# Performance work log

Hardware: AMD Instinct MI355X
Metric: run time of the kernel (lower is better)

## Reference

```python
import jax, jax.numpy as jnp
import numpy as np

B = 16
C = 80
LEVELS = [(128, 128, 8), (64, 64, 16), (32, 32, 32), (16, 16, 64), (8, 8, 128)]
TOPN = 1000
MIN_SCORE = 0.05
NMS_THR = 0.6
MAX_OBJ = 100


def setup_inputs() -> dict:
    key = jax.random.key(0)
    inp = {}
    for l, (H, W, s) in enumerate(LEVELS):
        key, k1, k2, k3 = jax.random.split(key, 4)
        inp[f"cls{l}"] = jax.random.uniform(k1, (B, H, W, C), jnp.float32)
        inp[f"reg{l}"] = jax.random.uniform(k2, (B, H, W, 4), jnp.float32) * 128.0
        inp[f"ctr{l}"] = jax.random.uniform(k3, (B, H, W, 1), jnp.float32)
        xs = (jnp.arange(W, dtype=jnp.float32) + 0.5) * s
        ys = (jnp.arange(H, dtype=jnp.float32) + 0.5) * s
        gx, gy = jnp.meshgrid(xs, ys)  # [H, W]
        pos = jnp.stack([gx, gy], axis=-1)  # [H, W, 2]
        inp[f"pos{l}"] = jnp.broadcast_to(pos, (B, H, W, 2))
    return inp


def _nms_one(scores, classes, bboxes):
    # scores [N], classes int32 [N], bboxes float [N, 4] (already int-truncated values)
    s = jnp.where(scores > MIN_SCORE, scores, -jnp.inf)  # score-threshold mask
    top_s, top_i = jax.lax.top_k(s, TOPN)  # sort descending, keep topn
    top_c = jax.lax.stop_gradient(classes[top_i].astype(jnp.float32))
    top_b = bboxes[top_i]
    valid = top_s > MIN_SCORE
    wh = top_b[:, 2:4] - top_b[:, 0:2]
    areas = jnp.clip(wh[:, 0] * wh[:, 1], 0.0001)
    ar = jnp.arange(TOPN)

    def body(i, suppressed):
        active = valid[i] & (~suppressed[i])
        b = top_b[i]
        tl = jnp.maximum(b[0:2], top_b[:, 0:2])
        br = jnp.minimum(b[2:4], top_b[:, 2:4])
        owh = jnp.clip(br - tl, 0.0)
        inter = owh[:, 0] * owh[:, 1]
        union = jnp.clip(areas[i] + areas - inter, 0.0001)
        iou = inter / union
        return suppressed | (active & (ar > i) & (iou >= NMS_THR))

    suppressed = jax.lax.fori_loop(0, TOPN, body, jnp.zeros((TOPN,), bool))
    keep = valid & (~suppressed)
    rank = jnp.cumsum(keep.astype(jnp.int32)) - 1
    # scatter kept detections (in score order) into first MAX_OBJ slots; slot MAX_OBJ is a dump
    idx = jnp.where(keep & (rank < MAX_OBJ), rank, MAX_OBJ)
    out_s = jnp.full((MAX_OBJ + 1,), -1.0, jnp.float32).at[idx].set(jnp.where(keep, top_s, -1.0))[:MAX_OBJ]
    out_c = jnp.full((MAX_OBJ + 1,), -1.0, jnp.float32).at[idx].set(jnp.where(keep, top_c, -1.0))[:MAX_OBJ]
    out_b = jnp.zeros((MAX_OBJ + 1, 4), jnp.float32).at[idx].set(jnp.where(keep[:, None], top_b, 0.0))[:MAX_OBJ]
    return out_s, out_c, out_b


def _forward(cls_list, reg_list, ctr_list, pos_list):
    ss, cc, bb = [], [], []
    for c, r, t, p in zip(cls_list, reg_list, ctr_list, pos_list):
        b = c.shape[0]
        c = c.reshape(b, -1, c.shape[-1])   # [B, HW, 80]
        r = r.reshape(b, -1, 4)             # [B, HW, 4]
        t = t.reshape(b, -1)                # [B, HW]
        p = p.reshape(b, -1, 2)             # [B, HW, 2]
        sc = jnp.sqrt(jnp.max(c, axis=2) * t)
        cl = jnp.argmax(c, axis=2).astype(jnp.int32)
        bmin = p - r[:, :, 0:2]
        bmax = p + r[:, :, 2:4]
        # torch .int() truncates toward zero; values are used as floats afterward
        box = jax.lax.stop_gradient(jnp.trunc(jnp.concatenate([bmin, bmax], axis=2)))
        ss.append(sc); cc.append(cl); bb.append(box)
    scores = jnp.concatenate(ss, axis=1)
    classes = jnp.concatenate(cc, axis=1)
    boxes = jnp.concatenate(bb, axis=1)
    return jax.vmap(_nms_one)(scores, classes, boxes)


def reference(cls0, cls1, cls2, cls3, cls4, reg0, reg1, reg2, reg3, reg4,
              ctr0, ctr1, ctr2, ctr3, ctr4, pos0, pos1, pos2, pos3, pos4):
    return _forward([cls0, cls1, cls2, cls3, cls4],
                    [reg0, reg1, reg2, reg3, reg4],
                    [ctr0, ctr1, ctr2, ctr3, ctr4],
                    [pos0, pos1, pos2, pos3, pos4])
```

## Files before the change

### kernel.cpp

```cpp
#include <hip/hip_runtime.h>
#include <stdint.h>

typedef unsigned int u32;
typedef unsigned long long u64;

#define NTOT 21824
#define NBATCH 16
#define TOPN 1000
#define MAXOBJ 100
#define CAP 2048
#define CAPC 8192

__global__ __launch_bounds__(256) void decode_kernel(
    const float* __restrict__ cls0, const float* __restrict__ cls1,
    const float* __restrict__ cls2, const float* __restrict__ cls3,
    const float* __restrict__ cls4,
    const float* __restrict__ ctr0, const float* __restrict__ ctr1,
    const float* __restrict__ ctr2, const float* __restrict__ ctr3,
    const float* __restrict__ ctr4,
    u32* __restrict__ keys, int* __restrict__ clsidx)
{
    int tid = threadIdx.x;
    int g = tid >> 2, j = tid & 3;
    int loc = blockIdx.x * 64 + g;
    int b = blockIdx.y;
    if (loc >= NTOT) return;
    const float *cp, *tp;
    if (loc < 16384)      { size_t o = (size_t)b*16384 + loc;          cp = cls0 + o*80; tp = ctr0 + o; }
    else if (loc < 20480) { size_t o = (size_t)b*4096  + (loc-16384);  cp = cls1 + o*80; tp = ctr1 + o; }
    else if (loc < 21504) { size_t o = (size_t)b*1024  + (loc-20480);  cp = cls2 + o*80; tp = ctr2 + o; }
    else if (loc < 21760) { size_t o = (size_t)b*256   + (loc-21504);  cp = cls3 + o*80; tp = ctr3 + o; }
    else                  { size_t o = (size_t)b*64    + (loc-21760);  cp = cls4 + o*80; tp = ctr4 + o; }

    const float4* c4 = (const float4*)cp;
    float maxv = -1.0f; int arg = 0;
#pragma unroll
    for (int q = 0; q < 5; ++q) {
        float4 v = c4[j + 4*q];
        int ch = 16*q + 4*j;
        if (v.x > maxv) { maxv = v.x; arg = ch;     }
        if (v.y > maxv) { maxv = v.y; arg = ch + 1; }
        if (v.z > maxv) { maxv = v.z; arg = ch + 2; }
        if (v.w > maxv) { maxv = v.w; arg = ch + 3; }
    }
#pragma unroll
    for (int d = 1; d <= 2; d <<= 1) {
        float ov = __shfl_xor(maxv, d);
        int   oa = __shfl_xor(arg, d);
        if (ov > maxv || (ov == maxv && oa < arg)) { maxv = ov; arg = oa; }
    }
    if (j == 0) {
        float score = sqrtf(maxv * (*tp));
        u32 key = (score > 0.05f) ? (__float_as_uint(score) | 0x80000000u) : 0u;
        size_t o = (size_t)b * NTOT + loc;
        keys[o] = key;
        clsidx[o] = arg;
    }
}

__global__ __launch_bounds__(1024) void pivot_kernel(
    const u32* __restrict__ keys,
    u64* __restrict__ cb, u64* __restrict__ cand2,
    u32* __restrict__ gcnt, u32* __restrict__ params,
    float* __restrict__ tscore, float* __restrict__ tcls, float4* __restrict__ tbox)
{
    __shared__ u32 h4[4][2048];
    __shared__ u32 s_wtot[16];
    __shared__ int s_tf;
    __shared__ u32 s_C, s_above, s_cnt;
    int b = blockIdx.x, tid = threadIdx.x;
    int lane = tid & 63, wave = tid >> 6, sub = wave & 3;
    const u32* kb = keys + (size_t)b * NTOT;
    u64* cbb = cb + (size_t)b * CAPC;
    u64* c2b = cand2 + (size_t)b * CAPC;

    for (int i = tid; i < TOPN; i += 1024) {
        size_t o = (size_t)b * TOPN + i;
        tscore[o] = -1.0f; tcls[o] = -1.0f;
        tbox[o] = make_float4(0.f, 0.f, 0.f, 0.f);
    }

    for (int i = tid; i < 4 * 2048; i += 1024) ((u32*)h4)[i] = 0;
    if (tid == 0) { s_tf = -1; s_cnt = 0; }
    __syncthreads();
    for (int i = tid; i < NTOT; i += 1024) {
        u32 k = kb[i];
        if (k) atomicAdd(&h4[sub][k >> 21], 1u);
    }
    __syncthreads();
    u32 h0 = h4[0][2*tid] + h4[1][2*tid] + h4[2][2*tid] + h4[3][2*tid];
    u32 h1 = h4[0][2*tid+1] + h4[1][2*tid+1] + h4[2][2*tid+1] + h4[3][2*tid+1];
    u32 x = h0 + h1;
#pragma unroll
    for (int off = 1; off < 64; off <<= 1) {
        u32 y = __shfl_down(x, off);
        if (lane + off < 64) x += y;
    }
    if (lane == 0) s_wtot[wave] = x;
    __syncthreads();
    u32 wsuf = 0, tot = 0;
    for (int w2 = 0; w2 < 16; ++w2) { u32 v = s_wtot[w2]; tot += v; if (w2 > wave) wsuf += v; }
    u32 suf0 = x + wsuf, suf1 = suf0 - h0;
    u32 target = (tot < TOPN) ? tot : TOPN;
    if (target > 0) {
        if (suf0 >= target) atomicMax(&s_tf, 2 * tid);
        if (suf1 >= target) atomicMax(&s_tf, 2 * tid + 1);
    }
    __syncthreads();
    int t0 = s_tf;
    if (target > 0) {
        if (2 * tid == t0)     { s_C = suf0; s_above = suf0 - h0; }
        if (2 * tid + 1 == t0) { s_C = suf1; s_above = suf1 - h1; }
    }
    __syncthreads();
    u32 C0 = (target > 0) ? s_C : 0;
    u32 above0 = (target > 0) ? s_above : 0;
    bool useCand = (C0 <= CAPC);

    for (int base = 0; base < NTOT; base += 1024) {
        int i = base + tid;
        u32 k = (i < NTOT) ? kb[i] : 0u;
        bool pass = (target > 0) && k && ((int)(k >> 21) >= t0);
        u64 mask = __ballot(pass);
        u32 wcnt = (u32)__popcll(mask);
        u32 wbase = 0;
        if (lane == 0 && wcnt) wbase = atomicAdd(&s_cnt, wcnt);
        wbase = __shfl(wbase, 0);
        if (pass) {
            u32 pos = wbase + (u32)__popcll(mask & ((1ull << lane) - 1ull));
            if (pos < CAPC) cbb[pos] = ((u64)k << 32) | (u32)(~i);
        }
    }
    __syncthreads();
    u32 C0g = s_cnt; (void)C0g;
    __syncthreads();
    if (tid == 0) s_cnt = 0;

    bool need2 = (target > 0 && C0 > CAP);
    int t1 = 0; u32 C1 = 0, above1 = 0;
    for (int i = tid; i < 4 * 2048; i += 1024) ((u32*)h4)[i] = 0;
    if (tid == 0) s_tf = -1;
    __syncthreads();
    if (need2) {
        if (useCand) {
            for (u32 i = tid; i < C0; i += 1024) {
                u32 k = (u32)(cbb[i] >> 32);
                if ((int)(k >> 21) == t0) atomicAdd(&h4[sub][(k >> 10) & 2047], 1u);
            }
        } else {
            for (int i = tid; i < NTOT; i += 1024) {
                u32 k = kb[i];
                if (k && (int)(k >> 21) == t0) atomicAdd(&h4[sub][(k >> 10) & 2047], 1u);
            }
        }
    }
    __syncthreads();
    {
        u32 g0 = h4[0][2*tid] + h4[1][2*tid] + h4[2][2*tid] + h4[3][2*tid];
        u32 g1 = h4[0][2*tid+1] + h4[1][2*tid+1] + h4[2][2*tid+1] + h4[3][2*tid+1];
        u32 x2 = g0 + g1;
#pragma unroll
        for (int off = 1; off < 64; off <<= 1) {
            u32 y = __shfl_down(x2, off);
            if (lane + off < 64) x2 += y;
        }
        if (lane == 0) s_wtot[wave] = x2;
        __syncthreads();
        u32 ws2 = 0;
        for (int w2 = wave + 1; w2 < 16; ++w2) ws2 += s_wtot[w2];
        u32 sa0 = x2 + ws2, sa1 = sa0 - g0;
        u32 need2c = target - above0;
        if (need2) {
            if (sa0 >= need2c) atomicMax(&s_tf, 2 * tid);
            if (sa1 >= need2c) atomicMax(&s_tf, 2 * tid + 1);
        }
        __syncthreads();
        t1 = s_tf;
        if (need2) {
            if (2 * tid == t1)     { s_C = above0 + sa0; s_above = above0 + sa0 - g0; }
            if (2 * tid + 1 == t1) { s_C = above0 + sa1; s_above = above0 + sa1 - g1; }
        }
        __syncthreads();
        if (need2) { C1 = s_C; above1 = s_above; }
    }

    bool need3 = (need2 && C1 > CAP);
    int t2 = 0;
    __syncthreads();
    for (int i = tid; i < 4 * 2048; i += 1024) ((u32*)h4)[i] = 0;
    if (tid == 0) s_tf = -1;
    __syncthreads();
    if (need3) {
        if (useCand) {
            for (u32 i = tid; i < C0; i += 1024) {
                u32 k = (u32)(cbb[i] >> 32);
                if ((int)(k >> 21) == t0 && (int)((k >> 10) & 2047) == t1)
                    atomicAdd(&h4[sub][k & 1023], 1u);
            }
        } else {
            for (int i = tid; i < NTOT; i += 1024) {
                u32 k = kb[i];
                if (k && (int)(k >> 21) == t0 && (int)((k >> 10) & 2047) == t1)
                    atomicAdd(&h4[sub][k & 1023], 1u);
            }
        }
    }
    __syncthreads();
    {
        u32 g0 = h4[0][2*tid] + h4[1][2*tid] + h4[2][2*tid] + h4[3][2*tid];
        u32 g1 = h4[0][2*tid+1] + h4[1][2*tid+1] + h4[2][2*tid+1] + h4[3][2*tid+1];
        u32 x3 = g0 + g1;
#pragma unroll
        for (int off = 1; off < 64; off <<= 1) {
            u32 y = __shfl_down(x3, off);
            if (lane + off < 64) x3 += y;
        }
        if (lane == 0) s_wtot[wave] = x3;
        __syncthreads();
        u32 ws3 = 0;
        for (int w2 = wave + 1; w2 < 16; ++w2) ws3 += s_wtot[w2];
        u32 sb0 = x3 + ws3, sb1 = sb0 - g0;
        if (need3) {
            u32 need3c = target - above1;
            if (sb0 >= need3c) atomicMax(&s_tf, 2 * tid);
            if (sb1 >= need3c) atomicMax(&s_tf, 2 * tid + 1);
        }
        __syncthreads();
        t2 = s_tf;
    }

    u32 P;
    if (target == 0) P = 0xFFFFFFFFu;
    else if (!need2) P = (u32)t0 << 21;
    else if (!need3) P = ((u32)t0 << 21) | ((u32)t1 << 10);
    else             P = ((u32)t0 << 21) | ((u32)t1 << 10) | (u32)t2;

    if (useCand) {
        u32 Cr = (C0 + 1023u) & ~1023u;
        for (u32 base = 0; base < Cr; base += 1024) {
            u32 i = base + tid;
            u64 e = 0; bool pass = false;
            if (i < C0 && target > 0) { e = cbb[i]; pass = ((u32)(e >> 32) >= P); }
            u64 mask = __ballot(pass);
            u32 wcnt = (u32)__popcll(mask);
            u32 wbase = 0;
            if (lane == 0 && wcnt) wbase = atomicAdd(&s_cnt, wcnt);
            wbase = __shfl(wbase, 0);
            if (pass) {
                u32 pos = wbase + (u32)__popcll(mask & ((1ull << lane) - 1ull));
                if (pos < CAPC) c2b[pos] = e;
            }
        }
    } else {
        for (int base = 0; base < NTOT; base += 1024) {
            int i = base + tid;
            u32 k = (i < NTOT) ? kb[i] : 0u;
            bool pass = (target > 0) && k && (k >= P);
            u64 mask = __ballot(pass);
            u32 wcnt = (u32)__popcll(mask);
            u32 wbase = 0;
            if (lane == 0 && wcnt) wbase = atomicAdd(&s_cnt, wcnt);
            wbase = __shfl(wbase, 0);
            if (pass) {
                u32 pos = wbase + (u32)__popcll(mask & ((1ull << lane) - 1ull));
                if (pos < CAPC) c2b[pos] = ((u64)k << 32) | (u32)(~i);
            }
        }
    }
    __syncthreads();
    if (tid == 0) {
        u32 M = s_cnt; if (M > CAPC) M = CAPC;
        gcnt[b * 32] = M;
        params[2 * b] = P;
        params[2 * b + 1] = target;
    }
}

__global__ __launch_bounds__(256) void rank_kernel(
    const u64* __restrict__ cand2, const u32* __restrict__ gcnt,
    const u32* __restrict__ params,
    const int* __restrict__ clsidx,
    const float* __restrict__ reg0, const float* __restrict__ reg1,
    const float* __restrict__ reg2, const float* __restrict__ reg3,
    const float* __restrict__ reg4,
    float* __restrict__ tscore, float* __restrict__ tcls, float4* __restrict__ tbox)
{
    int b = blockIdx.y;
    int lane = threadIdx.x & 63;
    u32 M = gcnt[b * 32]; if (M > CAPC) M = CAPC;
    u32 target = params[2 * b + 1];
    const u64* cb = cand2 + (size_t)b * CAPC;
    u32 Mr = (M + 63u) & ~63u;

    u32 wbase0 = blockIdx.x * 256 + (threadIdx.x & ~63u);
    for (u32 base = wbase0; base < M; base += 8 * 256) {
        u32 i0 = base + lane;
        bool val = (i0 < M);
        u64 e = val ? cb[i0] : ~0ull;
        u32 r = 0;
        for (u32 c0 = 0; c0 < Mr; c0 += 64) {
            u32 j = c0 + lane;
            u64 v = (j < M) ? cb[j] : 0ull;
            u32 vlo = (u32)v, vhi = (u32)(v >> 32);
#pragma unroll
            for (int s = 0; s < 64; ++s) {
                u32 lo = (u32)__builtin_amdgcn_readlane((int)vlo, s);
                u32 hi = (u32)__builtin_amdgcn_readlane((int)vhi, s);
                u64 vj = ((u64)hi << 32) | lo;
                r += (vj > e) ? 1u : 0u;
            }
        }
        if (val && r < target) {
            u32 k = (u32)(e >> 32);
            u32 loc = ~(u32)e;
            const float* rp; float st; u32 li; int wsh;
            if (loc < 16384u)      { li = loc;          wsh = 7; st = 8.f;   rp = reg0 + ((size_t)b*16384 + li)*4; }
            else if (loc < 20480u) { li = loc - 16384u; wsh = 6; st = 16.f;  rp = reg1 + ((size_t)b*4096  + li)*4; }
            else if (loc < 21504u) { li = loc - 20480u; wsh = 5; st = 32.f;  rp = reg2 + ((size_t)b*1024  + li)*4; }
            else if (loc < 21760u) { li = loc - 21504u; wsh = 4; st = 64.f;  rp = reg3 + ((size_t)b*256   + li)*4; }
            else                   { li = loc - 21760u; wsh = 3; st = 128.f; rp = reg4 + ((size_t)b*64    + li)*4; }
            u32 wx = li & ((1u << wsh) - 1u);
            u32 hy = li >> wsh;
            float px = ((float)wx + 0.5f) * st;
            float py = ((float)hy + 0.5f) * st;
            float4 rg = *(const float4*)rp;
            float4 bx;
            bx.x = truncf(px - rg.x); bx.y = truncf(py - rg.y);
            bx.z = truncf(px + rg.z); bx.w = truncf(py + rg.w);
            size_t src = (size_t)b * NTOT + loc;
            size_t o = (size_t)b * TOPN + r;
            tscore[o] = __uint_as_float(k & 0x7FFFFFFFu);
            tcls[o] = (float)clsidx[src];
            tbox[o] = bx;
        }
    }
}

__global__ __launch_bounds__(256) void iou_kernel(
    const float4* __restrict__ tbox, u64* __restrict__ sup)
{
    __shared__ float4 sbox[TOPN];
    int b = blockIdx.y;
    int tid = threadIdx.x, lane = tid & 63, wave = tid >> 6;
    const float4* tb = tbox + (size_t)b * TOPN;
    for (int i = tid; i < TOPN; i += 256) sbox[i] = tb[i];
    __syncthreads();
    int i = blockIdx.x * 4 + wave;
    float4 bi = sbox[i];
    float areai = fmaxf((bi.z - bi.x) * (bi.w - bi.y), 0.0001f);
    u64* row = sup + ((size_t)b * TOPN + i) * 16;
#pragma unroll
    for (int w = 0; w < 16; ++w) {
        int col = w * 64 + lane;
        bool bit = false;
        if (col < TOPN) {
            float4 bj = sbox[col];
            float areaj = fmaxf((bj.z - bj.x) * (bj.w - bj.y), 0.0001f);
            float tlx = fmaxf(bi.x, bj.x), tly = fmaxf(bi.y, bj.y);
            float brx = fminf(bi.z, bj.z), bry = fminf(bi.w, bj.w);
            float ow = fmaxf(brx - tlx, 0.f), oh = fmaxf(bry - tly, 0.f);
            float inter = ow * oh;
            float uni = fmaxf(areai + areaj - inter, 0.0001f);
            bit = (col > i) && (inter / uni >= 0.6f);
        }
        u64 m = __ballot(bit);
        if (lane == 0) row[w] = m;
    }
}

#define CHROWS 128
#define NCHUNK 8

__global__ __launch_bounds__(1024) void finalize_kernel(
    const float* __restrict__ tscore, const float* __restrict__ tcls,
    const float4* __restrict__ tbox, const u64* __restrict__ sup,
    float* __restrict__ out)
{
    __shared__ u64 mat[2][CHROWS * 16];
    __shared__ u32 validsh[TOPN];
    __shared__ u64 removed_sh[16];
    __shared__ u32 wpref[17];
    int b = blockIdx.x, tid = threadIdx.x;
    int wave = tid >> 6, lane = tid & 63;

    for (int i = tid; i < TOPN; i += 1024)
        validsh[i] = (tscore[(size_t)b * TOPN + i] > 0.05f) ? 1u : 0u;

    const u64* supb = sup + (size_t)b * TOPN * 16;
    for (int idx = tid; idx < CHROWS * 16; idx += 1024)
        mat[0][idx] = supb[idx];
    __syncthreads();

    u64 my = 0;
    if (wave == 0) {
#pragma unroll
        for (int w2 = 0; w2 < 16; ++w2) {
            int i = w2 * 64 + lane;
            bool v = (i < TOPN) ? (validsh[i] != 0) : false;
            u64 m = __ballot(v);
            if (lane == w2) my = ~m;
        }
    }

    for (int chunk = 0; chunk < NCHUNK; ++chunk) {
        if (wave > 0 && chunk + 1 < NCHUNK) {
            int nr = (chunk + 1 == NCHUNK - 1) ? (TOPN - (NCHUNK - 1) * CHROWS) : CHROWS;
            const u64* src = supb + (size_t)(chunk + 1) * CHROWS * 16;
            u64* dst = mat[(chunk + 1) & 1];
            for (int idx = tid - 64; idx < nr * 16; idx += 960)
                dst[idx] = src[idx];
        }
        if (wave == 0) {
            int r0 = chunk * CHROWS;
            int rows = (chunk == NCHUNK - 1) ? (TOPN - r0) : CHROWS;
            int lw = lane & 15;
            const u64* M = mat[chunk & 1];
            for (int sub = 0; sub < rows; sub += 64) {
                int w2 = (r0 + sub) >> 6;
                u64 cur = __shfl(my, w2);
                int nsub = rows - sub; if (nsub > 64) nsub = 64;
                const u64* R = M + sub * 16;
                int ngrp = nsub >> 3;
                u64 cme[8], cww[8];
#pragma unroll
                for (int g = 0; g < 8; ++g) { cme[g] = R[g*16 + lw]; cww[g] = R[g*16 + w2]; }
                for (int grp = 0; grp < ngrp; ++grp) {
                    u64 nme[8] = {0,0,0,0,0,0,0,0}, nww[8] = {0,0,0,0,0,0,0,0};
                    if (grp + 1 < ngrp) {
                        const u64* Rn = R + (grp + 1) * 128;
#pragma unroll
                        for (int g = 0; g < 8; ++g) { nme[g] = Rn[g*16 + lw]; nww[g] = Rn[g*16 + w2]; }
                    }
#pragma unroll
                    for (int g = 0; g < 8; ++g) {
                        int u = grp * 8 + g;
                        u64 bit = (cur >> u) & 1ull;
                        u64 act = bit - 1ull;
                        cur |= cww[g] & act;
                        my  |= cme[g] & act;
                    }
#pragma unroll
                    for (int g = 0; g < 8; ++g) { cme[g] = nme[g]; cww[g] = nww[g]; }
                }
            }
        }
        __syncthreads();
    }
    if (wave == 0) {
        if (lane < 16) removed_sh[lane] = my;
        u32 pc = (lane < 16) ? (u32)__popcll(~my) : 0u;
#pragma unroll
        for (int off = 1; off < 16; off <<= 1) {
            u32 y = __shfl_up(pc, off);
            if (lane >= off) pc += y;
        }
        if (lane < 16) wpref[lane + 1] = pc;
        if (lane == 0) wpref[0] = 0;
    }
    __syncthreads();

    float* out_s = out;
    float* out_c = out + NBATCH * MAXOBJ;
    float* out_b = out + 2 * NBATCH * MAXOBJ;
    if (tid < MAXOBJ)     { out_s[b * MAXOBJ + tid] = -1.f; out_c[b * MAXOBJ + tid] = -1.f; }
    if (tid < MAXOBJ * 4) out_b[b * MAXOBJ * 4 + tid] = 0.f;
    __syncthreads();
    if (tid < TOPN) {
        u64 kw = ~removed_sh[tid >> 6];
        if ((kw >> (tid & 63)) & 1ull) {
            int rank = (int)wpref[tid >> 6] + (int)__popcll(kw & ((1ull << (tid & 63)) - 1ull));
            if (rank < MAXOBJ) {
                size_t o = (size_t)b * TOPN + tid;
                out_s[b * MAXOBJ + rank] = tscore[o];
                out_c[b * MAXOBJ + rank] = tcls[o];
                ((float4*)out_b)[b * MAXOBJ + rank] = tbox[o];
            }
        }
    }
}

extern "C" void kernel_launch(void* const* d_in, const int* in_sizes, int n_in,
                              void* d_out, int out_size, void* d_ws, size_t ws_size,
                              hipStream_t stream) {
    (void)in_sizes; (void)n_in; (void)out_size; (void)ws_size;
    const float* cls[5]; const float* reg[5]; const float* ctr[5];
    for (int l = 0; l < 5; ++l) {
        cls[l] = (const float*)d_in[4 * l + 0];
        reg[l] = (const float*)d_in[4 * l + 1];
        ctr[l] = (const float*)d_in[4 * l + 2];
    }
    char* w = (char*)d_ws;
    u32*    keys   = (u32*)(w + 0);
    int*    clsidx = (int*)(w + 1396736);
    u64*    cb     = (u64*)(w + 2793472);
    u64*    cand2  = (u64*)(w + 3842048);
    float*  tscore = (float*)(w + 8380416);
    float*  tcls   = (float*)(w + 8444416);
    float4* tbox   = (float4*)(w + 8508416);
    u64*    sup    = (u64*)(w + 8764416);
    u32*    gcnt   = (u32*)(w + 9944064);
    u32*    params = (u32*)(w + 9946112);

    decode_kernel<<<dim3((NTOT + 63) / 64, NBATCH), 256, 0, stream>>>(
        cls[0], cls[1], cls[2], cls[3], cls[4],
        ctr[0], ctr[1], ctr[2], ctr[3], ctr[4],
        keys, clsidx);
    pivot_kernel<<<NBATCH, 1024, 0, stream>>>(keys, cb, cand2, gcnt, params,
                                              tscore, tcls, tbox);
    rank_kernel<<<dim3(8, NBATCH), 256, 0, stream>>>(cand2, gcnt, params, clsidx,
                                                     reg[0], reg[1], reg[2], reg[3], reg[4],
                                                     tscore, tcls, tbox);
    iou_kernel<<<dim3(TOPN / 4, NBATCH), 256, 0, stream>>>(tbox, sup);
    finalize_kernel<<<NBATCH, 1024, 0, stream>>>(tscore, tcls, tbox, sup, (float*)d_out);
}
```

Before: 283.4 us.

## Fuse pivot, rank, IoU and NMS finalize into one per-batch mega kernel

Merges the pivot-selection, candidate ranking, IoU bitmask and greedy suppression stages into a single 1024-thread block per batch image. The top-1000 boxes, scores and classes stay in shared memory, and IoU bitmask chunks are computed by 15 waves while wave 0 runs the serial suppression scan on the previous chunk. This removes three kernel launches and the global round trips for the intermediate arrays and the suppression matrix. The decode kernel also becomes grid-stride with a fixed 96 blocks per batch. In exchange, ranking and IoU now run on only 16 blocks, which cuts parallelism for those stages sharply.

```diff
diff --git a/kernel.cpp b/kernel.cpp
--- a/kernel.cpp
+++ b/kernel.cpp
@@ -10,6 +10,8 @@
 #define MAXOBJ 100
 #define CAP 2048
 #define CAPC 8192
+#define CHROWS 64
+#define NCHUNK 16
 
 __global__ __launch_bounds__(256) void decode_kernel(
     const float* __restrict__ cls0, const float* __restrict__ cls1,
@@ -22,74 +24,107 @@
 {
     int tid = threadIdx.x;
     int g = tid >> 2, j = tid & 3;
-    int loc = blockIdx.x * 64 + g;
     int b = blockIdx.y;
-    if (loc >= NTOT) return;
-    const float *cp, *tp;
-    if (loc < 16384)      { size_t o = (size_t)b*16384 + loc;          cp = cls0 + o*80; tp = ctr0 + o; }
-    else if (loc < 20480) { size_t o = (size_t)b*4096  + (loc-16384);  cp = cls1 + o*80; tp = ctr1 + o; }
-    else if (loc < 21504) { size_t o = (size_t)b*1024  + (loc-20480);  cp = cls2 + o*80; tp = ctr2 + o; }
-    else if (loc < 21760) { size_t o = (size_t)b*256   + (loc-21504);  cp = cls3 + o*80; tp = ctr3 + o; }
-    else                  { size_t o = (size_t)b*64    + (loc-21760);  cp = cls4 + o*80; tp = ctr4 + o; }
-
-    const float4* c4 = (const float4*)cp;
-    float maxv = -1.0f; int arg = 0;
-#pragma unroll
-    for (int q = 0; q < 5; ++q) {
-        float4 v = c4[j + 4*q];
-        int ch = 16*q + 4*j;
-        if (v.x > maxv) { maxv = v.x; arg = ch;     }
-        if (v.y > maxv) { maxv = v.y; arg = ch + 1; }
-        if (v.z > maxv) { maxv = v.z; arg = ch + 2; }
-        if (v.w > maxv) { maxv = v.w; arg = ch + 3; }
-    }
-#pragma unroll
-    for (int d = 1; d <= 2; d <<= 1) {
-        float ov = __shfl_xor(maxv, d);
-        int   oa = __shfl_xor(arg, d);
-        if (ov > maxv || (ov == maxv && oa < arg)) { maxv = ov; arg = oa; }
-    }
-    if (j == 0) {
-        float score = sqrtf(maxv * (*tp));
-        u32 key = (score > 0.05f) ? (__float_as_uint(score) | 0x80000000u) : 0u;
-        size_t o = (size_t)b * NTOT + loc;
-        keys[o] = key;
-        clsidx[o] = arg;
+    for (int bx = blockIdx.x; bx < NTOT / 64; bx += gridDim.x) {
+        int loc = bx * 64 + g;
+        const float *cp, *tp;
+        if (loc < 16384)      { size_t o = (size_t)b*16384 + loc;          cp = cls0 + o*80; tp = ctr0 + o; }
+        else if (loc < 20480) { size_t o = (size_t)b*4096  + (loc-16384);  cp = cls1 + o*80; tp = ctr1 + o; }
+        else if (loc < 21504) { size_t o = (size_t)b*1024  + (loc-20480);  cp = cls2 + o*80; tp = ctr2 + o; }
+        else if (loc < 21760) { size_t o = (size_t)b*256   + (loc-21504);  cp = cls3 + o*80; tp = ctr3 + o; }
+        else                  { size_t o = (size_t)b*64    + (loc-21760);  cp = cls4 + o*80; tp = ctr4 + o; }
+
+        const float4* c4 = (const float4*)cp;
+        float maxv = -1.0f; int arg = 0;
+#pragma unroll
+        for (int q = 0; q < 5; ++q) {
+            float4 v = c4[j + 4*q];
+            int ch = 16*q + 4*j;
+            if (v.x > maxv) { maxv = v.x; arg = ch;     }
+            if (v.y > maxv) { maxv = v.y; arg = ch + 1; }
+            if (v.z > maxv) { maxv = v.z; arg = ch + 2; }
+            if (v.w > maxv) { maxv = v.w; arg = ch + 3; }
+        }
+#pragma unroll
+        for (int d = 1; d <= 2; d <<= 1) {
+            float ov = __shfl_xor(maxv, d);
+            int   oa = __shfl_xor(arg, d);
+            if (ov > maxv || (ov == maxv && oa < arg)) { maxv = ov; arg = oa; }
+        }
+        if (j == 0) {
+            float score = sqrtf(maxv * (*tp));
+            u32 key = (score > 0.05f) ? (__float_as_uint(score) | 0x80000000u) : 0u;
+            size_t o = (size_t)b * NTOT + loc;
+            keys[o] = key;
+            clsidx[o] = arg;
+        }
     }
 }
 
-__global__ __launch_bounds__(1024) void pivot_kernel(
-    const u32* __restrict__ keys,
-    u64* __restrict__ cb, u64* __restrict__ cand2,
-    u32* __restrict__ gcnt, u32* __restrict__ params,
-    float* __restrict__ tscore, float* __restrict__ tcls, float4* __restrict__ tbox)
+__device__ __forceinline__ void compute_chunk(
+    int c, int idx, int nw, int lane,
+    const float4* sbox, const float* sarea, u64* matc)
 {
-    __shared__ u32 h4[4][2048];
+    int r0 = c * CHROWS;
+    int rows = (TOPN - r0 < CHROWS) ? (TOPN - r0) : CHROWS;
+    for (int r = idx; r < rows; r += nw) {
+        int row = r0 + r;
+        float4 bi = sbox[row];
+        float areai = sarea[row];
+        int wstart = row >> 6;
+        if (lane < wstart) matc[r * 16 + lane] = 0;
+        for (int w = wstart; w < 16; ++w) {
+            int col = w * 64 + lane;
+            bool bit = false;
+            if (col < TOPN && col > row) {
+                float4 bj = sbox[col];
+                float areaj = sarea[col];
+                float tlx = fmaxf(bi.x, bj.x), tly = fmaxf(bi.y, bj.y);
+                float brx = fminf(bi.z, bj.z), bry = fminf(bi.w, bj.w);
+                float ow = fmaxf(brx - tlx, 0.f), oh = fmaxf(bry - tly, 0.f);
+                float inter = ow * oh;
+                float uni = fmaxf(areai + areaj - inter, 0.0001f);
+                bit = (inter / uni >= 0.6f);
+            }
+            u64 m = __ballot(bit);
+            if (lane == w) matc[r * 16 + w] = m;
+        }
+    }
+}
+
+__global__ __launch_bounds__(1024) void mega_kernel(
+    const u32* __restrict__ keys, const int* __restrict__ clsidx,
+    const float* __restrict__ reg0, const float* __restrict__ reg1,
+    const float* __restrict__ reg2, const float* __restrict__ reg3,
+    const float* __restrict__ reg4,
+    u64* __restrict__ cb, u64* __restrict__ cb2,
+    float* __restrict__ out)
+{
+    __shared__ __align__(16) u64 shbuf[4096];
+    __shared__ u64 mat[2][CHROWS * 16];
     __shared__ u32 s_wtot[16];
     __shared__ int s_tf;
     __shared__ u32 s_C, s_above, s_cnt;
+    __shared__ u64 removed_sh[16];
+    __shared__ u32 wpref[17];
+
+    u32* h4flat = (u32*)shbuf;
     int b = blockIdx.x, tid = threadIdx.x;
-    int lane = tid & 63, wave = tid >> 6, sub = wave & 3;
+    int lane = tid & 63, wave = tid >> 6, hsub = wave & 3;
     const u32* kb = keys + (size_t)b * NTOT;
     u64* cbb = cb + (size_t)b * CAPC;
-    u64* c2b = cand2 + (size_t)b * CAPC;
-
-    for (int i = tid; i < TOPN; i += 1024) {
-        size_t o = (size_t)b * TOPN + i;
-        tscore[o] = -1.0f; tcls[o] = -1.0f;
-        tbox[o] = make_float4(0.f, 0.f, 0.f, 0.f);
-    }
-
-    for (int i = tid; i < 4 * 2048; i += 1024) ((u32*)h4)[i] = 0;
+    u64* c2b = cb2 + (size_t)b * CAPC;
+
+    for (int i = tid; i < 8192; i += 1024) h4flat[i] = 0;
     if (tid == 0) { s_tf = -1; s_cnt = 0; }
     __syncthreads();
     for (int i = tid; i < NTOT; i += 1024) {
         u32 k = kb[i];
-        if (k) atomicAdd(&h4[sub][k >> 21], 1u);
-    }
-    __syncthreads();
-    u32 h0 = h4[0][2*tid] + h4[1][2*tid] + h4[2][2*tid] + h4[3][2*tid];
-    u32 h1 = h4[0][2*tid+1] + h4[1][2*tid+1] + h4[2][2*tid+1] + h4[3][2*tid+1];
+        if (k) atomicAdd(&h4flat[hsub * 2048 + (k >> 21)], 1u);
+    }
+    __syncthreads();
+    u32 h0 = h4flat[2*tid] + h4flat[2048 + 2*tid] + h4flat[4096 + 2*tid] + h4flat[6144 + 2*tid];
+    u32 h1 = h4flat[2*tid+1] + h4flat[2048 + 2*tid+1] + h4flat[4096 + 2*tid+1] + h4flat[6144 + 2*tid+1];
     u32 x = h0 + h1;
 #pragma unroll
     for (int off = 1; off < 64; off <<= 1) {
@@ -132,32 +167,30 @@
         }
     }
     __syncthreads();
-    u32 C0g = s_cnt; (void)C0g;
-    __syncthreads();
     if (tid == 0) s_cnt = 0;
 
     bool need2 = (target > 0 && C0 > CAP);
     int t1 = 0; u32 C1 = 0, above1 = 0;
-    for (int i = tid; i < 4 * 2048; i += 1024) ((u32*)h4)[i] = 0;
+    for (int i = tid; i < 8192; i += 1024) h4flat[i] = 0;
     if (tid == 0) s_tf = -1;
     __syncthreads();
     if (need2) {
         if (useCand) {
             for (u32 i = tid; i < C0; i += 1024) {
                 u32 k = (u32)(cbb[i] >> 32);
-                if ((int)(k >> 21) == t0) atomicAdd(&h4[sub][(k >> 10) & 2047], 1u);
+                if ((int)(k >> 21) == t0) atomicAdd(&h4flat[hsub * 2048 + ((k >> 10) & 2047)], 1u);
             }
         } else {
             for (int i = tid; i < NTOT; i += 1024) {
                 u32 k = kb[i];
-                if (k && (int)(k >> 21) == t0) atomicAdd(&h4[sub][(k >> 10) & 2047], 1u);
+                if (k && (int)(k >> 21) == t0) atomicAdd(&h4flat[hsub * 2048 + ((k >> 10) & 2047)], 1u);
             }
         }
     }
     __syncthreads();
     {
-        u32 g0 = h4[0][2*tid] + h4[1][2*tid] + h4[2][2*tid] + h4[3][2*tid];
-        u32 g1 = h4[0][2*tid+1] + h4[1][2*tid+1] + h4[2][2*tid+1] + h4[3][2*tid+1];
+        u32 g0 = h4flat[2*tid] + h4flat[2048 + 2*tid] + h4flat[4096 + 2*tid] + h4flat[6144 + 2*tid];
+        u32 g1 = h4flat[2*tid+1] + h4flat[2048 + 2*tid+1] + h4flat[4096 + 2*tid+1] + h4flat[6144 + 2*tid+1];
         u32 x2 = g0 + g1;
 #pragma unroll
         for (int off = 1; off < 64; off <<= 1) {
@@ -187,7 +220,7 @@
     bool need3 = (need2 && C1 > CAP);
     int t2 = 0;
     __syncthreads();
-    for (int i = tid; i < 4 * 2048; i += 1024) ((u32*)h4)[i] = 0;
+    for (int i = tid; i < 8192; i += 1024) h4flat[i] = 0;
     if (tid == 0) s_tf = -1;
     __syncthreads();
     if (need3) {
@@ -195,20 +228,20 @@
             for (u32 i = tid; i < C0; i += 1024) {
                 u32 k = (u32)(cbb[i] >> 32);
                 if ((int)(k >> 21) == t0 && (int)((k >> 10) & 2047) == t1)
-                    atomicAdd(&h4[sub][k & 1023], 1u);
+                    atomicAdd(&h4flat[hsub * 2048 + (k & 1023)], 1u);
             }
         } else {
             for (int i = tid; i < NTOT; i += 1024) {
                 u32 k = kb[i];
                 if (k && (int)(k >> 21) == t0 && (int)((k >> 10) & 2047) == t1)
-                    atomicAdd(&h4[sub][k & 1023], 1u);
+                    atomicAdd(&h4flat[hsub * 2048 + (k & 1023)], 1u);
             }
         }
     }
     __syncthreads();
     {
-        u32 g0 = h4[0][2*tid] + h4[1][2*tid] + h4[2][2*tid] + h4[3][2*tid];
-        u32 g1 = h4[0][2*tid+1] + h4[1][2*tid+1] + h4[2][2*tid+1] + h4[3][2*tid+1];
+        u32 g0 = h4flat[2*tid] + h4flat[2048 + 2*tid] + h4flat[4096 + 2*tid] + h4flat[6144 + 2*tid];
+        u32 g1 = h4flat[2*tid+1] + h4flat[2048 + 2*tid+1] + h4flat[4096 + 2*tid+1] + h4flat[6144 + 2*tid+1];
         u32 x3 = g0 + g1;
 #pragma unroll
         for (int off = 1; off < 64; off <<= 1) {
@@ -235,6 +268,7 @@
     else if (!need3) P = ((u32)t0 << 21) | ((u32)t1 << 10);
     else             P = ((u32)t0 << 21) | ((u32)t1 << 10) | (u32)t2;
 
+    __syncthreads();
     if (useCand) {
         u32 Cr = (C0 + 1023u) & ~1023u;
         for (u32 base = 0; base < Cr; base += 1024) {
@@ -268,39 +302,28 @@
         }
     }
     __syncthreads();
-    if (tid == 0) {
-        u32 M = s_cnt; if (M > CAPC) M = CAPC;
-        gcnt[b * 32] = M;
-        params[2 * b] = P;
-        params[2 * b + 1] = target;
-    }
-}
-
-__global__ __launch_bounds__(256) void rank_kernel(
-    const u64* __restrict__ cand2, const u32* __restrict__ gcnt,
-    const u32* __restrict__ params,
-    const int* __restrict__ clsidx,
-    const float* __restrict__ reg0, const float* __restrict__ reg1,
-    const float* __restrict__ reg2, const float* __restrict__ reg3,
-    const float* __restrict__ reg4,
-    float* __restrict__ tscore, float* __restrict__ tcls, float4* __restrict__ tbox)
-{
-    int b = blockIdx.y;
-    int lane = threadIdx.x & 63;
-    u32 M = gcnt[b * 32]; if (M > CAPC) M = CAPC;
-    u32 target = params[2 * b + 1];
-    const u64* cb = cand2 + (size_t)b * CAPC;
+    u32 M = s_cnt; if (M > CAPC) M = CAPC;
+
+    float4* sbox  = (float4*)shbuf;
+    float*  sarea = (float*)((char*)shbuf + 16000);
+    float*  sscore= (float*)((char*)shbuf + 20000);
+    float*  scls  = (float*)((char*)shbuf + 24000);
+    __syncthreads();
+    for (int i = tid; i < TOPN; i += 1024) {
+        sscore[i] = -1.0f; scls[i] = -1.0f;
+        sbox[i] = make_float4(0.f, 0.f, 0.f, 0.f);
+    }
+    __syncthreads();
+
     u32 Mr = (M + 63u) & ~63u;
-
-    u32 wbase0 = blockIdx.x * 256 + (threadIdx.x & ~63u);
-    for (u32 base = wbase0; base < M; base += 8 * 256) {
+    for (u32 base = wave * 64; base < M; base += 16 * 64) {
         u32 i0 = base + lane;
         bool val = (i0 < M);
-        u64 e = val ? cb[i0] : ~0ull;
+        u64 e = val ? c2b[i0] : ~0ull;
         u32 r = 0;
         for (u32 c0 = 0; c0 < Mr; c0 += 64) {
-            u32 j = c0 + lane;
-            u64 v = (j < M) ? cb[j] : 0ull;
+            u32 jj = c0 + lane;
+            u64 v = (jj < M) ? c2b[jj] : 0ull;
             u32 vlo = (u32)v, vhi = (u32)(v >> 32);
 #pragma unroll
             for (int s = 0; s < 64; ++s) {
@@ -327,68 +350,17 @@
             float4 bx;
             bx.x = truncf(px - rg.x); bx.y = truncf(py - rg.y);
             bx.z = truncf(px + rg.z); bx.w = truncf(py + rg.w);
-            size_t src = (size_t)b * NTOT + loc;
-            size_t o = (size_t)b * TOPN + r;
-            tscore[o] = __uint_as_float(k & 0x7FFFFFFFu);
-            tcls[o] = (float)clsidx[src];
-            tbox[o] = bx;
-        }
-    }
-}
-
-__global__ __launch_bounds__(256) void iou_kernel(
-    const float4* __restrict__ tbox, u64* __restrict__ sup)
-{
-    __shared__ float4 sbox[TOPN];
-    int b = blockIdx.y;
-    int tid = threadIdx.x, lane = tid & 63, wave = tid >> 6;
-    const float4* tb = tbox + (size_t)b * TOPN;
-    for (int i = tid; i < TOPN; i += 256) sbox[i] = tb[i];
-    __syncthreads();
-    int i = blockIdx.x * 4 + wave;
-    float4 bi = sbox[i];
-    float areai = fmaxf((bi.z - bi.x) * (bi.w - bi.y), 0.0001f);
-    u64* row = sup + ((size_t)b * TOPN + i) * 16;
-#pragma unroll
-    for (int w = 0; w < 16; ++w) {
-        int col = w * 64 + lane;
-        bool bit = false;
-        if (col < TOPN) {
-            float4 bj = sbox[col];
-            float areaj = fmaxf((bj.z - bj.x) * (bj.w - bj.y), 0.0001f);
-            float tlx = fmaxf(bi.x, bj.x), tly = fmaxf(bi.y, bj.y);
-            float brx = fminf(bi.z, bj.z), bry = fminf(bi.w, bj.w);
-            float ow = fmaxf(brx - tlx, 0.f), oh = fmaxf(bry - tly, 0.f);
-            float inter = ow * oh;
-            float uni = fmaxf(areai + areaj - inter, 0.0001f);
-            bit = (col > i) && (inter / uni >= 0.6f);
-        }
-        u64 m = __ballot(bit);
-        if (lane == 0) row[w] = m;
-    }
-}
-
-#define CHROWS 128
-#define NCHUNK 8
-
-__global__ __launch_bounds__(1024) void finalize_kernel(
-    const float* __restrict__ tscore, const float* __restrict__ tcls,
-    const float4* __restrict__ tbox, const u64* __restrict__ sup,
-    float* __restrict__ out)
-{
-    __shared__ u64 mat[2][CHROWS * 16];
-    __shared__ u32 validsh[TOPN];
-    __shared__ u64 removed_sh[16];
-    __shared__ u32 wpref[17];
-    int b = blockIdx.x, tid = threadIdx.x;
-    int wave = tid >> 6, lane = tid & 63;
-
-    for (int i = tid; i < TOPN; i += 1024)
-        validsh[i] = (tscore[(size_t)b * TOPN + i] > 0.05f) ? 1u : 0u;
-
-    const u64* supb = sup + (size_t)b * TOPN * 16;
-    for (int idx = tid; idx < CHROWS * 16; idx += 1024)
-        mat[0][idx] = supb[idx];
+            sscore[r] = __uint_as_float(k & 0x7FFFFFFFu);
+            scls[r] = (float)clsidx[(size_t)b * NTOT + loc];
+            sbox[r] = bx;
+        }
+    }
+    __syncthreads();
+
+    for (int i = tid; i < TOPN; i += 1024) {
+        float4 bb = sbox[i];
+        sarea[i] = fmaxf((bb.z - bb.x) * (bb.w - bb.y), 0.0001f);
+    }
     __syncthreads();
 
     u64 my = 0;
@@ -396,52 +368,44 @@
 #pragma unroll
         for (int w2 = 0; w2 < 16; ++w2) {
             int i = w2 * 64 + lane;
-            bool v = (i < TOPN) ? (validsh[i] != 0) : false;
+            bool v = (i < TOPN) ? (sscore[i] > 0.05f) : false;
             u64 m = __ballot(v);
             if (lane == w2) my = ~m;
         }
     }
+    compute_chunk(0, wave, 16, lane, sbox, sarea, mat[0]);
+    __syncthreads();
 
     for (int chunk = 0; chunk < NCHUNK; ++chunk) {
-        if (wave > 0 && chunk + 1 < NCHUNK) {
-            int nr = (chunk + 1 == NCHUNK - 1) ? (TOPN - (NCHUNK - 1) * CHROWS) : CHROWS;
-            const u64* src = supb + (size_t)(chunk + 1) * CHROWS * 16;
-            u64* dst = mat[(chunk + 1) & 1];
-            for (int idx = tid - 64; idx < nr * 16; idx += 960)
-                dst[idx] = src[idx];
-        }
+        if (wave > 0 && chunk + 1 < NCHUNK)
+            compute_chunk(chunk + 1, wave - 1, 15, lane, sbox, sarea, mat[(chunk + 1) & 1]);
         if (wave == 0) {
             int r0 = chunk * CHROWS;
             int rows = (chunk == NCHUNK - 1) ? (TOPN - r0) : CHROWS;
             int lw = lane & 15;
-            const u64* M = mat[chunk & 1];
-            for (int sub = 0; sub < rows; sub += 64) {
-                int w2 = (r0 + sub) >> 6;
-                u64 cur = __shfl(my, w2);
-                int nsub = rows - sub; if (nsub > 64) nsub = 64;
-                const u64* R = M + sub * 16;
-                int ngrp = nsub >> 3;
-                u64 cme[8], cww[8];
-#pragma unroll
-                for (int g = 0; g < 8; ++g) { cme[g] = R[g*16 + lw]; cww[g] = R[g*16 + w2]; }
-                for (int grp = 0; grp < ngrp; ++grp) {
-                    u64 nme[8] = {0,0,0,0,0,0,0,0}, nww[8] = {0,0,0,0,0,0,0,0};
-                    if (grp + 1 < ngrp) {
-                        const u64* Rn = R + (grp + 1) * 128;
-#pragma unroll
-                        for (int g = 0; g < 8; ++g) { nme[g] = Rn[g*16 + lw]; nww[g] = Rn[g*16 + w2]; }
-                    }
-#pragma unroll
-                    for (int g = 0; g < 8; ++g) {
-                        int u = grp * 8 + g;
-                        u64 bit = (cur >> u) & 1ull;
-                        u64 act = bit - 1ull;
-                        cur |= cww[g] & act;
-                        my  |= cme[g] & act;
-                    }
-#pragma unroll
-                    for (int g = 0; g < 8; ++g) { cme[g] = nme[g]; cww[g] = nww[g]; }
+            const u64* R = mat[chunk & 1];
+            u64 cur = __shfl(my, chunk);
+            int ngrp = rows >> 3;
+            u64 cme[8], cww[8];
+#pragma unroll
+            for (int g2 = 0; g2 < 8; ++g2) { cme[g2] = R[g2*16 + lw]; cww[g2] = R[g2*16 + chunk]; }
+            for (int grp = 0; grp < ngrp; ++grp) {
+                u64 nme[8] = {0,0,0,0,0,0,0,0}, nww[8] = {0,0,0,0,0,0,0,0};
+                if (grp + 1 < ngrp) {
+                    const u64* Rn = R + (grp + 1) * 128;
+#pragma unroll
+                    for (int g2 = 0; g2 < 8; ++g2) { nme[g2] = Rn[g2*16 + lw]; nww[g2] = Rn[g2*16 + chunk]; }
                 }
+#pragma unroll
+                for (int g2 = 0; g2 < 8; ++g2) {
+                    int u = grp * 8 + g2;
+                    u64 bit = (cur >> u) & 1ull;
+                    u64 act = bit - 1ull;
+                    cur |= cww[g2] & act;
+                    my  |= cme[g2] & act;
+                }
+#pragma unroll
+                for (int g2 = 0; g2 < 8; ++g2) { cme[g2] = nme[g2]; cww[g2] = nww[g2]; }
             }
         }
         __syncthreads();
@@ -470,10 +434,9 @@
         if ((kw >> (tid & 63)) & 1ull) {
             int rank = (int)wpref[tid >> 6] + (int)__popcll(kw & ((1ull << (tid & 63)) - 1ull));
             if (rank < MAXOBJ) {
-                size_t o = (size_t)b * TOPN + tid;
-                out_s[b * MAXOBJ + rank] = tscore[o];
-                out_c[b * MAXOBJ + rank] = tcls[o];
-                ((float4*)out_b)[b * MAXOBJ + rank] = tbox[o];
+                out_s[b * MAXOBJ + rank] = sscore[tid];
+                out_c[b * MAXOBJ + rank] = scls[tid];
+                ((float4*)out_b)[b * MAXOBJ + rank] = sbox[tid];
             }
         }
     }
@@ -490,26 +453,17 @@
         ctr[l] = (const float*)d_in[4 * l + 2];
     }
     char* w = (char*)d_ws;
-    u32*    keys   = (u32*)(w + 0);
-    int*    clsidx = (int*)(w + 1396736);
-    u64*    cb     = (u64*)(w + 2793472);
-    u64*    cand2  = (u64*)(w + 3842048);
-    float*  tscore = (float*)(w + 8380416);
-    float*  tcls   = (float*)(w + 8444416);
-    float4* tbox   = (float4*)(w + 8508416);
-    u64*    sup    = (u64*)(w + 8764416);
-    u32*    gcnt   = (u32*)(w + 9944064);
-    u32*    params = (u32*)(w + 9946112);
-
-    decode_kernel<<<dim3((NTOT + 63) / 64, NBATCH), 256, 0, stream>>>(
+    u32* keys   = (u32*)(w + 0);
+    int* clsidx = (int*)(w + 1396736);
+    u64* cb     = (u64*)(w + 2793472);
+    u64* cb2    = (u64*)(w + 3842048);
+
+    decode_kernel<<<dim3(96, NBATCH), 256, 0, stream>>>(
         cls[0], cls[1], cls[2], cls[3], cls[4],
         ctr[0], ctr[1], ctr[2], ctr[3], ctr[4],
         keys, clsidx);
-    pivot_kernel<<<NBATCH, 1024, 0, stream>>>(keys, cb, cand2, gcnt, params,
-                                              tscore, tcls, tbox);
-    rank_kernel<<<dim3(8, NBATCH), 256, 0, stream>>>(cand2, gcnt, params, clsidx,
-                                                     reg[0], reg[1], reg[2], reg[3], reg[4],
-                                                     tscore, tcls, tbox);
-    iou_kernel<<<dim3(TOPN / 4, NBATCH), 256, 0, stream>>>(tbox, sup);
-    finalize_kernel<<<NBATCH, 1024, 0, stream>>>(tscore, tcls, tbox, sup, (float*)d_out);
+    mega_kernel<<<NBATCH, 1024, 0, stream>>>(
+        keys, clsidx,
+        reg[0], reg[1], reg[2], reg[3], reg[4],
+        cb, cb2, (float*)d_out);
 }
```

Result: slower. 422.9 us (+49.2%).
